# Kernel tuning notes

Measured on AMD Instinct MI355X. Metric: run time of the kernel, lower is better.

The kernel has to match this reference:

```python
import jax, jax.numpy as jnp
import numpy as np

STATE, EMB, VOC, T = 1024, 512, 32000, 512

def setup_inputs() -> dict:
    key = jax.random.key(0)
    ks = jax.random.split(key, 12)
    u = 1.0 / np.sqrt(STATE)  # torch LSTMCell init scale
    return {
        "l_hid_state": jax.random.normal(ks[0], (STATE,), jnp.float32),
        "l_cell_state": jax.random.normal(ks[1], (STATE,), jnp.float32),
        "target_ids": jax.random.randint(ks[2], (T,), 0, VOC),
        "emb_table": jax.random.normal(ks[3], (VOC + 1, EMB), jnp.float32),
        "W_ih": jax.random.uniform(ks[4], (4 * STATE, EMB + 2 * STATE), jnp.float32, -u, u),
        "W_hh": jax.random.uniform(ks[5], (4 * STATE, STATE), jnp.float32, -u, u),
        "b_ih": jax.random.uniform(ks[6], (4 * STATE,), jnp.float32, -u, u),
        "b_hh": jax.random.uniform(ks[7], (4 * STATE,), jnp.float32, -u, u),
        "X": jax.random.normal(ks[8], (VOC, STATE), jnp.float32),
        "Y": jax.random.normal(ks[9], (VOC, EMB), jnp.float32),
        "Z": jax.random.normal(ks[10], (VOC, 2 * STATE), jnp.float32),
    }


def reference(l_hid_state, l_cell_state, target_ids, emb_table, W_ih, W_hh, b_ih, b_hh, X, Y, Z):
    E = emb_table.shape[1]
    # torch loop iterates [target_ids[-1]] + target_ids[:-1] -> shift right
    shifted = jnp.roll(target_ids, 1)
    embs = emb_table[shifted]                      # [T, E]
    fixed = jnp.concatenate([l_hid_state, l_cell_state])  # [2S], constant every step
    # precompute input-side gate preactivations for all steps: [T, 4S]
    gates_x = embs @ W_ih[:, :E].T + (W_ih[:, E:] @ fixed + b_ih)[None, :]

    def step(carry, gx):
        h, c = carry
        gates = gx + h @ W_hh.T + b_hh
        i, f, g, o = jnp.split(gates, 4)
        i = jax.nn.sigmoid(i)
        f = jax.nn.sigmoid(f)
        g = jnp.tanh(g)
        o = jax.nn.sigmoid(o)
        c = f * c + i * g
        h = o * jnp.tanh(c)
        return (h, c), h

    _, hs = jax.lax.scan(step, (l_hid_state, l_cell_state), gates_x)  # hs: [T, S]
    # scores_t = X @ h_t + Y @ emb_t + Z @ fixed
    scores = hs @ X.T + embs @ Y.T + (Z @ fixed)[None, :]  # [T, VOC]
    return scores
```

## Files before the change

kernel.cpp:

```cpp
#include <hip/hip_runtime.h>
#include <stdint.h>

#define T_STEPS 512

typedef __bf16 bf16x8v __attribute__((ext_vector_type(8)));
typedef float f32x4 __attribute__((ext_vector_type(4)));
typedef unsigned short u16x8 __attribute__((ext_vector_type(8)));

__device__ __forceinline__ unsigned short f2bf(float f) {
    unsigned u = __float_as_uint(f);
    return (unsigned short)((u + 0x7fffu + ((u >> 16) & 1u)) >> 16);
}

typedef __attribute__((address_space(1))) void as1_void;
typedef __attribute__((address_space(3))) void as3_void;

__device__ __forceinline__ void async16(const void* g, void* l) {
    __builtin_amdgcn_global_load_lds((as1_void*)(void*)g, (as3_void*)l, 16, 0, 0);
}
__device__ __forceinline__ void async4(const void* g, void* l) {
    __builtin_amdgcn_global_load_lds((as1_void*)(void*)g, (as3_void*)l, 4, 0, 0);
}

__global__ void k_rowdot(const float* __restrict__ M, int rs, int coff,
                         const float* __restrict__ h0, const float* __restrict__ c0,
                         const float* __restrict__ b1, const float* __restrict__ b2,
                         float* __restrict__ out, int nrows) {
    int wave = threadIdx.x >> 6, lane = threadIdx.x & 63;
    int r = blockIdx.x * 4 + wave;
    if (r >= nrows) return;
    const float* row = M + (long)r * rs + coff;
    float acc = 0.f;
#pragma unroll
    for (int it = 0; it < 8; ++it) {
        int k = it * 256 + lane * 4;
        float4 w = *(const float4*)(row + k);
        const float4* xp = (k < 1024) ? (const float4*)(h0 + k)
                                      : (const float4*)(c0 + (k - 1024));
        float4 x = *xp;
        acc += w.x * x.x + w.y * x.y + w.z * x.z + w.w * x.w;
    }
#pragma unroll
    for (int off = 32; off; off >>= 1) acc += __shfl_xor(acc, off, 64);
    if (lane == 0) {
        if (b1) acc += b1[r];
        if (b2) acc += b2[r];
        out[r] = acc;
    }
}

__global__ void k_embs(const int* __restrict__ ids, const float* __restrict__ emb,
                       unsigned short* __restrict__ U) {
    int t = blockIdx.x, j = threadIdx.x;
    int id = ids[(t + T_STEPS - 1) & (T_STEPS - 1)];
    float2 v = *(const float2*)(emb + (long)id * 512 + j * 2);
    ushort2 s;
    s.x = f2bf(v.x); s.y = f2bf(v.y);
    *(ushort2*)(U + (long)t * 1536 + 1024 + j * 2) = s;
}

__global__ void k_convW(const float* __restrict__ Wih, unsigned short* __restrict__ Wb) {
    int i = blockIdx.x * 256 + threadIdx.x;
    int r = i >> 7, c4 = i & 127;
    float4 f = *(const float4*)(Wih + (long)r * 2560 + c4 * 4);
    ushort4 s;
    s.x = f2bf(f.x); s.y = f2bf(f.y); s.z = f2bf(f.z); s.w = f2bf(f.w);
    *(ushort4*)(Wb + (long)r * 512 + c4 * 4) = s;
}

__global__ void k_convXY(const float* __restrict__ X, const float* __restrict__ Y,
                         unsigned short* __restrict__ V) {
    long i = (long)blockIdx.x * 256 + threadIdx.x;
    const long NX = (long)32000 * 256;
    if (i < NX) {
        long v = i >> 8; int c4 = (int)(i & 255);
        float4 f = *(const float4*)(X + v * 1024 + c4 * 4);
        ushort4 s;
        s.x = f2bf(f.x); s.y = f2bf(f.y); s.z = f2bf(f.z); s.w = f2bf(f.w);
        *(ushort4*)(V + v * 1536 + c4 * 4) = s;
    } else {
        i -= NX;
        long v = i >> 7; int c4 = (int)(i & 127);
        float4 f = *(const float4*)(Y + v * 512 + c4 * 4);
        ushort4 s;
        s.x = f2bf(f.x); s.y = f2bf(f.y); s.z = f2bf(f.z); s.w = f2bf(f.w);
        *(ushort4*)(V + v * 1536 + 1024 + c4 * 4) = s;
    }
}

__global__ __launch_bounds__(256) void k_gemm_bt(
    const unsigned short* __restrict__ A, int lda,
    const unsigned short* __restrict__ B, int ldb,
    float* __restrict__ C, int ldc,
    const float* __restrict__ bias, int K) {
    __shared__ __align__(16) unsigned short As[128 * 32];
    __shared__ __align__(16) unsigned short Bs[128 * 32];
    const int tid = threadIdx.x;
    const long m0 = (long)blockIdx.y * 128, n0 = (long)blockIdx.x * 128;
    const int wave = tid >> 6, lane = tid & 63;
    const int wm = (wave >> 1) * 64, wn = (wave & 1) * 64;
    const int lm = lane & 15, lk = (lane >> 4) * 8;
    const int r0 = tid >> 2, r1 = (tid + 256) >> 2, kc = (tid & 3) * 8;
    const unsigned short* Ab = A + m0 * lda;
    const unsigned short* Bb = B + n0 * ldb;

    f32x4 acc[4][4];
#pragma unroll
    for (int i = 0; i < 4; ++i)
#pragma unroll
        for (int j = 0; j < 4; ++j) {
            f32x4 z = {0.f, 0.f, 0.f, 0.f};
            acc[i][j] = z;
        }

    for (int k0 = 0; k0 < K; k0 += 32) {
        async16(Ab + (long)r0 * lda + k0 + kc, &As[tid * 8]);
        async16(Ab + (long)r1 * lda + k0 + kc, &As[(tid + 256) * 8]);
        async16(Bb + (long)r0 * ldb + k0 + kc, &Bs[tid * 8]);
        async16(Bb + (long)r1 * ldb + k0 + kc, &Bs[(tid + 256) * 8]);
        __syncthreads();
        bf16x8v af[4], bfr[4];
#pragma unroll
        for (int t = 0; t < 4; ++t) af[t] = *(const bf16x8v*)&As[(wm + t * 16 + lm) * 32 + lk];
#pragma unroll
        for (int t = 0; t < 4; ++t) bfr[t] = *(const bf16x8v*)&Bs[(wn + t * 16 + lm) * 32 + lk];
#pragma unroll
        for (int i = 0; i < 4; ++i)
#pragma unroll
            for (int j = 0; j < 4; ++j)
                acc[i][j] = __builtin_amdgcn_mfma_f32_16x16x32_bf16(af[i], bfr[j], acc[i][j], 0, 0, 0);
        __syncthreads();
    }
    const int quad = lane >> 4;
#pragma unroll
    for (int j = 0; j < 4; ++j) {
        long col = n0 + wn + j * 16 + lm;
        float bv = bias ? bias[col] : 0.0f;
#pragma unroll
        for (int i = 0; i < 4; ++i)
#pragma unroll
            for (int rg = 0; rg < 4; ++rg) {
                long row = m0 + wm + i * 16 + quad * 4 + rg;
                C[row * (long)ldc + col] = acc[i][j][rg] + bv;
            }
    }
}

__global__ __launch_bounds__(256) void k_scan(
    const float* __restrict__ Whh, const float* __restrict__ gx,
    const float* __restrict__ h0, const float* __restrict__ c0,
    unsigned long long* __restrict__ hx, unsigned short* __restrict__ U) {
    __shared__ __align__(16) float hs[1024];
    __shared__ __align__(16) float gxb[32 * 16];
    __shared__ float gv[16];
    const int b = blockIdx.x, tid = threadIdx.x;
    const int lr = tid >> 4, seg = tid & 15;

    const float* wrow = Whh + (long)((lr >> 2) * 1024 + b * 4 + (lr & 3)) * 1024;
    f32x4 wv[16];
#pragma unroll
    for (int u = 0; u < 8; ++u) {
        wv[2 * u]     = *(const f32x4*)(wrow + u * 128 + seg * 8);
        wv[2 * u + 1] = *(const f32x4*)(wrow + u * 128 + seg * 8 + 4);
    }
    float cA = 0.f, cB = 0.f;
    if (tid < 2) { cA = c0[b * 4 + 2 * tid]; cB = c0[b * 4 + 2 * tid + 1]; }

    for (int t = 0; t < T_STEPS; ++t) {
        if ((t & 31) == 0) {
            __syncthreads();
            int c = tid;
            async4(gx + (long)(t + (c >> 4)) * 4096 + ((c & 15) >> 2) * 1024 + b * 4 + (c & 3), &gxb[c]);
            c = tid + 256;
            async4(gx + (long)(t + (c >> 4)) * 4096 + ((c & 15) >> 2) * 1024 + b * 4 + (c & 3), &gxb[c]);
        }
        if (t == 0) {
            float4 hv = *(const float4*)(h0 + tid * 4);
            *(float4*)&hs[tid * 4] = hv;
        } else {
            const unsigned long long* src = hx + (long)(t & 1) * 512 + tid * 2;
            unsigned long long w0, w1;
            do { w0 = __hip_atomic_load(src,     __ATOMIC_RELAXED, __HIP_MEMORY_SCOPE_AGENT); }
            while ((unsigned)(w0 >> 32) != (unsigned)t);
            do { w1 = __hip_atomic_load(src + 1, __ATOMIC_RELAXED, __HIP_MEMORY_SCOPE_AGENT); }
            while ((unsigned)(w1 >> 32) != (unsigned)t);
            union { unsigned u; _Float16 h[2]; } p0, p1;
            p0.u = (unsigned)w0; p1.u = (unsigned)w1;
            hs[tid * 4 + 0] = (float)p0.h[0];
            hs[tid * 4 + 1] = (float)p0.h[1];
            hs[tid * 4 + 2] = (float)p1.h[0];
            hs[tid * 4 + 3] = (float)p1.h[1];
        }
        __syncthreads();

        float acc = 0.f;
#pragma unroll
        for (int u = 0; u < 8; ++u) {
            const f32x4 ha = *(const f32x4*)&hs[u * 128 + seg * 8];
            const f32x4 hb = *(const f32x4*)&hs[u * 128 + seg * 8 + 4];
            const f32x4 wa = wv[2 * u], wb = wv[2 * u + 1];
            acc += wa[0] * ha[0] + wa[1] * ha[1] + wa[2] * ha[2] + wa[3] * ha[3]
                 + wb[0] * hb[0] + wb[1] * hb[1] + wb[2] * hb[2] + wb[3] * hb[3];
        }
#pragma unroll
        for (int off = 1; off < 16; off <<= 1) acc += __shfl_xor(acc, off, 64);
        if (seg == 0) gv[lr] = acc;
        __syncthreads();

        if (tid < 2) {
            const int sl = (t & 31) * 16;
            union { unsigned u; _Float16 h[2]; } pk;
            unsigned short ub[2];
            float cc[2] = {cA, cB};
#pragma unroll
            for (int q = 0; q < 2; ++q) {
                const int j = 2 * tid + q;
                float ig = gv[j]      + gxb[sl + j];
                float fg = gv[4 + j]  + gxb[sl + 4 + j];
                float gg = gv[8 + j]  + gxb[sl + 8 + j];
                float og = gv[12 + j] + gxb[sl + 12 + j];
                float si = 1.f / (1.f + expf(-ig));
                float sf = 1.f / (1.f + expf(-fg));
                float so = 1.f / (1.f + expf(-og));
                float cn = sf * cc[q] + si * tanhf(gg);
                float hn = so * tanhf(cn);
                cc[q] = cn;
                pk.h[q] = (_Float16)hn;
                ub[q] = f2bf(hn);
            }
            cA = cc[0]; cB = cc[1];
            *(ushort2*)(U + (long)t * 1536 + b * 4 + 2 * tid) = *(ushort2*)ub;
            unsigned long long word = (unsigned long long)pk.u
                                    | ((unsigned long long)(unsigned)(t + 1) << 32);
            __hip_atomic_store(&hx[(long)((t + 1) & 1) * 512 + b * 2 + tid], word,
                               __ATOMIC_RELAXED, __HIP_MEMORY_SCOPE_AGENT);
        }
    }
}

extern "C" void kernel_launch(void* const* d_in, const int* in_sizes, int n_in,
                              void* d_out, int out_size, void* d_ws, size_t ws_size,
                              hipStream_t stream) {
    const float* h0  = (const float*)d_in[0];
    const float* c0  = (const float*)d_in[1];
    const int*   ids = (const int*)d_in[2];
    const float* emb = (const float*)d_in[3];
    const float* Wih = (const float*)d_in[4];
    const float* Whh = (const float*)d_in[5];
    const float* bih = (const float*)d_in[6];
    const float* bhh = (const float*)d_in[7];
    const float* X   = (const float*)d_in[8];
    const float* Y   = (const float*)d_in[9];
    const float* Z   = (const float*)d_in[10];
    float* out = (float*)d_out;

    char* ws = (char*)d_ws;
    size_t off = 0;
    auto take = [&](size_t bytes) -> char* {
        char* p = ws + off;
        off = (off + bytes + 511) & ~(size_t)511;
        return p;
    };
    unsigned long long* hx = (unsigned long long*)take(2 * 512 * 8);
    float* wf            = (float*)take(4096 * 4);
    float* zf            = (float*)take(32000 * 4);
    unsigned short* U    = (unsigned short*)take((size_t)512 * 1536 * 2);
    unsigned short* Wihb = (unsigned short*)take((size_t)4096 * 512 * 2);
    float* gatesx        = (float*)take((size_t)512 * 4096 * 4);
    unsigned short* Vbf  = (unsigned short*)take((size_t)32000 * 1536 * 2);
    (void)in_sizes; (void)n_in; (void)out_size; (void)ws_size;

    hipMemsetAsync(hx, 0, 2 * 512 * 8, stream);
    k_rowdot<<<1024, 256, 0, stream>>>(Wih, 2560, 512, h0, c0, bih, bhh, wf, 4096);
    k_rowdot<<<8000, 256, 0, stream>>>(Z, 2048, 0, h0, c0, nullptr, nullptr, zf, 32000);
    k_embs<<<512, 256, 0, stream>>>(ids, emb, U);
    k_convW<<<2048, 256, 0, stream>>>(Wih, Wihb);
    k_gemm_bt<<<dim3(32, 4), 256, 0, stream>>>(U + 1024, 1536, Wihb, 512, gatesx, 4096, wf, 512);
    k_convXY<<<48000, 256, 0, stream>>>(X, Y, Vbf);
    k_scan<<<256, 256, 0, stream>>>(Whh, gatesx, h0, c0, hx, U);
    k_gemm_bt<<<dim3(250, 4), 256, 0, stream>>>(U, 1536, Vbf, 1536, out, 32000, zf, 1536);
}
```

Before: 2.322 ms.

## Add global step counter barrier and parallelize LSTM gate nonlinearity across 16 lanes

Replaces the per-thread spin on tagged h words with a single-thread spin on a global arrival counter, followed by a block barrier and a combined poll of both words. The gate activations are spread over 16 lanes, with tanh written as 2*sigmoid(2x)-1, and the results are gathered with shuffles. One lane then publishes the packed h words and increments the counter. The aim is to cut polling traffic on the hidden-state buffer and shorten the serial gate math on the recurrent critical path. In exchange it adds an extra atomic and a wait for memory completion to every step, plus s_sleep latency in the spin.

```diff
diff --git a/kernel.cpp b/kernel.cpp
--- a/kernel.cpp
+++ b/kernel.cpp
@@ -146,10 +146,11 @@
     }
 }
 
-__global__ __launch_bounds__(256) void k_scan(
+__global__ __launch_bounds__(256, 1) void k_scan(
     const float* __restrict__ Whh, const float* __restrict__ gx,
     const float* __restrict__ h0, const float* __restrict__ c0,
-    unsigned long long* __restrict__ hx, unsigned short* __restrict__ U) {
+    unsigned long long* __restrict__ hx, unsigned* __restrict__ cnt,
+    unsigned short* __restrict__ U) {
     __shared__ __align__(16) float hs[1024];
     __shared__ __align__(16) float gxb[32 * 16];
     __shared__ float gv[16];
@@ -163,8 +164,7 @@
         wv[2 * u]     = *(const f32x4*)(wrow + u * 128 + seg * 8);
         wv[2 * u + 1] = *(const f32x4*)(wrow + u * 128 + seg * 8 + 4);
     }
-    float cA = 0.f, cB = 0.f;
-    if (tid < 2) { cA = c0[b * 4 + 2 * tid]; cB = c0[b * 4 + 2 * tid + 1]; }
+    float cst = (tid < 4) ? c0[b * 4 + tid] : 0.f;
 
     for (int t = 0; t < T_STEPS; ++t) {
         if ((t & 31) == 0) {
@@ -178,12 +178,20 @@
             float4 hv = *(const float4*)(h0 + tid * 4);
             *(float4*)&hs[tid * 4] = hv;
         } else {
+            if (tid == 0) {
+                const unsigned need = (unsigned)t << 8;
+                while (__hip_atomic_load(cnt, __ATOMIC_RELAXED, __HIP_MEMORY_SCOPE_AGENT) < need) {
+                    __builtin_amdgcn_s_sleep(1);
+                }
+            }
+            __syncthreads();
             const unsigned long long* src = hx + (long)(t & 1) * 512 + tid * 2;
             unsigned long long w0, w1;
-            do { w0 = __hip_atomic_load(src,     __ATOMIC_RELAXED, __HIP_MEMORY_SCOPE_AGENT); }
-            while ((unsigned)(w0 >> 32) != (unsigned)t);
-            do { w1 = __hip_atomic_load(src + 1, __ATOMIC_RELAXED, __HIP_MEMORY_SCOPE_AGENT); }
-            while ((unsigned)(w1 >> 32) != (unsigned)t);
+            const unsigned tt = (unsigned)t;
+            do {
+                w0 = __hip_atomic_load(src,     __ATOMIC_RELAXED, __HIP_MEMORY_SCOPE_AGENT);
+                w1 = __hip_atomic_load(src + 1, __ATOMIC_RELAXED, __HIP_MEMORY_SCOPE_AGENT);
+            } while ((((unsigned)(w0 >> 32) ^ tt) | ((unsigned)(w1 >> 32) ^ tt)) != 0u);
             union { unsigned u; _Float16 h[2]; } p0, p1;
             p0.u = (unsigned)w0; p1.u = (unsigned)w1;
             hs[tid * 4 + 0] = (float)p0.h[0];
@@ -207,33 +215,41 @@
         if (seg == 0) gv[lr] = acc;
         __syncthreads();
 
-        if (tid < 2) {
+        if (tid < 16) {
             const int sl = (t & 31) * 16;
-            union { unsigned u; _Float16 h[2]; } pk;
-            unsigned short ub[2];
-            float cc[2] = {cA, cB};
-#pragma unroll
-            for (int q = 0; q < 2; ++q) {
-                const int j = 2 * tid + q;
-                float ig = gv[j]      + gxb[sl + j];
-                float fg = gv[4 + j]  + gxb[sl + 4 + j];
-                float gg = gv[8 + j]  + gxb[sl + 8 + j];
-                float og = gv[12 + j] + gxb[sl + 12 + j];
-                float si = 1.f / (1.f + expf(-ig));
-                float sf = 1.f / (1.f + expf(-fg));
-                float so = 1.f / (1.f + expf(-og));
-                float cn = sf * cc[q] + si * tanhf(gg);
-                float hn = so * tanhf(cn);
-                cc[q] = cn;
-                pk.h[q] = (_Float16)hn;
-                ub[q] = f2bf(hn);
-            }
-            cA = cc[0]; cB = cc[1];
-            *(ushort2*)(U + (long)t * 1536 + b * 4 + 2 * tid) = *(ushort2*)ub;
-            unsigned long long word = (unsigned long long)pk.u
-                                    | ((unsigned long long)(unsigned)(t + 1) << 32);
-            __hip_atomic_store(&hx[(long)((t + 1) & 1) * 512 + b * 2 + tid], word,
-                               __ATOMIC_RELAXED, __HIP_MEMORY_SCOPE_AGENT);
+            float x = gv[tid] + gxb[sl + tid];
+            const bool isg = (tid & 12) == 8;
+            float y = isg ? (x + x) : x;
+            float s = 1.f / (1.f + expf(-y));
+            float v = isg ? (s + s - 1.f) : s;
+            const int cell = tid & 3;
+            float iv = __shfl(v, cell,      64);
+            float fv = __shfl(v, cell + 4,  64);
+            float gg = __shfl(v, cell + 8,  64);
+            float ov = __shfl(v, cell + 12, 64);
+            float hn = 0.f;
+            if (tid < 4) {
+                float cn = fv * cst + iv * gg;
+                cst = cn;
+                hn = ov * tanhf(cn);
+                U[(long)t * 1536 + b * 4 + tid] = f2bf(hn);
+            }
+            float h1 = __shfl(hn, 1, 64);
+            float h2 = __shfl(hn, 2, 64);
+            float h3 = __shfl(hn, 3, 64);
+            if (tid == 0) {
+                union { unsigned u; _Float16 h[2]; } pa, pb;
+                pa.h[0] = (_Float16)hn; pa.h[1] = (_Float16)h1;
+                pb.h[0] = (_Float16)h2; pb.h[1] = (_Float16)h3;
+                const unsigned long long tg = (unsigned long long)(unsigned)(t + 1) << 32;
+                unsigned long long* dst = hx + (long)((t + 1) & 1) * 512 + b * 2;
+                __hip_atomic_store(dst,     (unsigned long long)pa.u | tg,
+                                   __ATOMIC_RELAXED, __HIP_MEMORY_SCOPE_AGENT);
+                __hip_atomic_store(dst + 1, (unsigned long long)pb.u | tg,
+                                   __ATOMIC_RELAXED, __HIP_MEMORY_SCOPE_AGENT);
+                asm volatile("s_waitcnt vmcnt(0)" ::: "memory");
+                __hip_atomic_fetch_add(cnt, 1u, __ATOMIC_RELAXED, __HIP_MEMORY_SCOPE_AGENT);
+            }
         }
     }
 }
@@ -261,7 +277,8 @@
         off = (off + bytes + 511) & ~(size_t)511;
         return p;
     };
-    unsigned long long* hx = (unsigned long long*)take(2 * 512 * 8);
+    unsigned long long* hx = (unsigned long long*)take(2 * 512 * 8 + 256);
+    unsigned* cnt        = (unsigned*)((char*)hx + 2 * 512 * 8);
     float* wf            = (float*)take(4096 * 4);
     float* zf            = (float*)take(32000 * 4);
     unsigned short* U    = (unsigned short*)take((size_t)512 * 1536 * 2);
@@ -270,13 +287,13 @@
     unsigned short* Vbf  = (unsigned short*)take((size_t)32000 * 1536 * 2);
     (void)in_sizes; (void)n_in; (void)out_size; (void)ws_size;
 
-    hipMemsetAsync(hx, 0, 2 * 512 * 8, stream);
+    hipMemsetAsync(hx, 0, 2 * 512 * 8 + 256, stream);
     k_rowdot<<<1024, 256, 0, stream>>>(Wih, 2560, 512, h0, c0, bih, bhh, wf, 4096);
     k_rowdot<<<8000, 256, 0, stream>>>(Z, 2048, 0, h0, c0, nullptr, nullptr, zf, 32000);
     k_embs<<<512, 256, 0, stream>>>(ids, emb, U);
     k_convW<<<2048, 256, 0, stream>>>(Wih, Wihb);
     k_gemm_bt<<<dim3(32, 4), 256, 0, stream>>>(U + 1024, 1536, Wihb, 512, gatesx, 4096, wf, 512);
     k_convXY<<<48000, 256, 0, stream>>>(X, Y, Vbf);
-    k_scan<<<256, 256, 0, stream>>>(Whh, gatesx, h0, c0, hx, U);
+    k_scan<<<256, 256, 0, stream>>>(Whh, gatesx, h0, c0, hx, cnt, U);
     k_gemm_bt<<<dim3(250, 4), 256, 0, stream>>>(U, 1536, Vbf, 1536, out, 32000, zf, 1536);
 }
```

After: 3.441 ms. +48.2%, slower.
